# Kernel tuning notes

Hardware: AMD Instinct MI355X
Metric: run time of the kernel (lower is better)

## Reference

```python
import jax, jax.numpy as jnp
import numpy as np

N = 4096
FIN = 512
HID = 256
NCLS = 2
NE = 131072

def _glorot(key, fan_in, fan_out):
    r = np.sqrt(6.0 / (fan_in + fan_out))
    return jax.random.uniform(key, (fan_in, fan_out), jnp.float32, -r, r)

def setup_inputs() -> dict:
    key = jax.random.key(0)
    ks = jax.random.split(key, 16)
    X = jax.random.normal(ks[0], (N, FIN), jnp.float32)
    adj_rows = jax.random.randint(ks[1], (NE,), 0, N, jnp.int32)
    adj_cols = jax.random.randint(ks[2], (NE,), 0, N, jnp.int32)
    adj_vals = jax.random.uniform(ks[3], (NE,), jnp.float32)
    W_shared = _glorot(ks[4], FIN, HID)
    W_iv = _glorot(ks[5], HID, HID)
    W_c = _glorot(ks[6], HID, HID)
    W_r = _glorot(ks[7], HID, HID)
    Wg_iv = _glorot(ks[8], HID, HID)
    Wg_c = _glorot(ks[9], HID, HID)
    Wg_r = _glorot(ks[10], HID, HID)
    lin_W = _glorot(ks[11], 2 * HID, NCLS)
    lin_b = jnp.zeros((NCLS,), jnp.float32)
    return {"X": X, "adj_rows": adj_rows, "adj_cols": adj_cols, "adj_vals": adj_vals,
            "W_shared": W_shared, "W_iv": W_iv, "W_c": W_c, "W_r": W_r,
            "Wg_iv": Wg_iv, "Wg_c": Wg_c, "Wg_r": Wg_r, "lin_W": lin_W, "lin_b": lin_b}

def _spmm(rows, cols, vals, m):
    # sparse.mm(adj, m): out[i] = sum_{e: rows[e]==i} vals[e] * m[cols[e]]
    return jax.ops.segment_sum(vals[:, None] * m[cols], rows, num_segments=N)

def _gcn(x, rows, cols, vals, W):
    # dropout is identity in eval mode
    return jax.nn.relu(_spmm(rows, cols, vals, x @ W))

def _graphite(x, r1, r2, W):
    h = x @ W
    return jax.nn.relu(r1 @ (r1.T @ h) + r2 @ (r2.T @ h))

def reference(X, adj_rows, adj_cols, adj_vals, W_shared, W_iv, W_c, W_r, Wg_iv, Wg_c, Wg_r, lin_W, lin_b):
    h = _gcn(X, adj_rows, adj_cols, adj_vals, W_shared)
    z_iv0 = _gcn(h, adj_rows, adj_cols, adj_vals, W_iv)
    z_c0 = _gcn(h, adj_rows, adj_cols, adj_vals, W_c)
    z_r0 = _gcn(h, adj_rows, adj_cols, adj_vals, W_r)
    z_iv_rec0 = z_iv0 @ z_iv0.T
    z_c_rec0 = z_c0 @ z_c0.T
    z_r_rec0 = z_r0 @ z_r0.T
    A_dense = jnp.zeros((N, N), jnp.float32).at[adj_rows, adj_cols].add(adj_vals)
    z_iv = _graphite(z_iv0, A_dense, jax.nn.sigmoid(z_iv_rec0), Wg_iv)
    z_c = _graphite(z_c0, A_dense, jax.nn.sigmoid(z_c_rec0), Wg_c)
    z_r = _graphite(z_r0, A_dense, jax.nn.sigmoid(z_r_rec0), Wg_r)
    z_iv_rec = z_iv @ z_iv.T
    z_c_rec = z_c @ z_c.T
    z_r_rec = z_r @ z_r.T
    concat = jnp.concatenate([z_iv, z_c], axis=1)
    pred_T = jax.nn.log_softmax(concat @ lin_W + lin_b, axis=1)
    mi_total_loss = jnp.array(0.0, jnp.float32)
    return (z_iv, z_iv_rec, z_c, z_c_rec, z_r, z_r_rec, mi_total_loss, pred_T)
```

## Files before the change

### kernel.cpp

```cpp
#include <hip/hip_runtime.h>

#define Nn   4096
#define FINd 512
#define HIDd 256
#define NEd  131072

typedef unsigned short u16;
typedef __bf16 bf16x8 __attribute__((ext_vector_type(8)));
typedef float floatx4 __attribute__((ext_vector_type(4)));

__device__ __forceinline__ float bf2f(u16 u) {
  union { unsigned int i; float f; } v; v.i = ((unsigned int)u) << 16; return v.f;
}
__device__ __forceinline__ u16 f2bf(float f) {
  union { unsigned int i; float f; } v; v.f = f;
  unsigned int x = v.i;
  return (u16)((x + 0x7FFFu + ((x >> 16) & 1u)) >> 16);
}

#define GLDS(gp, lp) __builtin_amdgcn_global_load_lds( \
    (__attribute__((address_space(1))) unsigned int*)(void*)(gp), \
    (__attribute__((address_space(3))) unsigned int*)(lp), 16, 0, 0)

#define GATH4(EP, M, F, AX, AY, AZ, AW, E)                                     \
  {                                                                            \
    int2 c0 = (EP)[E]; int2 c1 = (EP)[(E) + 1];                                \
    int2 c2 = (EP)[(E) + 2]; int2 c3 = (EP)[(E) + 3];                          \
    ushort4 m0 = *(const ushort4*)((M) + (size_t)c0.x * HIDd + (F));           \
    ushort4 m1 = *(const ushort4*)((M) + (size_t)c1.x * HIDd + (F));           \
    ushort4 m2 = *(const ushort4*)((M) + (size_t)c2.x * HIDd + (F));           \
    ushort4 m3 = *(const ushort4*)((M) + (size_t)c3.x * HIDd + (F));           \
    float v0 = __int_as_float(c0.y), v1 = __int_as_float(c1.y);                \
    float v2 = __int_as_float(c2.y), v3 = __int_as_float(c3.y);                \
    AX = fmaf(v3, bf2f(m3.x), fmaf(v2, bf2f(m2.x), fmaf(v1, bf2f(m1.x), fmaf(v0, bf2f(m0.x), AX)))); \
    AY = fmaf(v3, bf2f(m3.y), fmaf(v2, bf2f(m2.y), fmaf(v1, bf2f(m1.y), fmaf(v0, bf2f(m0.y), AY)))); \
    AZ = fmaf(v3, bf2f(m3.z), fmaf(v2, bf2f(m2.z), fmaf(v1, bf2f(m1.z), fmaf(v0, bf2f(m0.z), AZ)))); \
    AW = fmaf(v3, bf2f(m3.w), fmaf(v2, bf2f(m2.w), fmaf(v1, bf2f(m1.w), fmaf(v0, bf2f(m0.w), AW)))); \
  }

#define GATH8(EP, M, F, AX, AY, AZ, AW, E)                                     \
  {                                                                            \
    int2 c0 = (EP)[E];       int2 c1 = (EP)[(E) + 1];                          \
    int2 c2 = (EP)[(E) + 2]; int2 c3 = (EP)[(E) + 3];                          \
    int2 c4 = (EP)[(E) + 4]; int2 c5 = (EP)[(E) + 5];                          \
    int2 c6 = (EP)[(E) + 6]; int2 c7 = (EP)[(E) + 7];                          \
    ushort4 m0 = *(const ushort4*)((M) + (size_t)c0.x * HIDd + (F));           \
    ushort4 m1 = *(const ushort4*)((M) + (size_t)c1.x * HIDd + (F));           \
    ushort4 m2 = *(const ushort4*)((M) + (size_t)c2.x * HIDd + (F));           \
    ushort4 m3 = *(const ushort4*)((M) + (size_t)c3.x * HIDd + (F));           \
    ushort4 m4 = *(const ushort4*)((M) + (size_t)c4.x * HIDd + (F));           \
    ushort4 m5 = *(const ushort4*)((M) + (size_t)c5.x * HIDd + (F));           \
    ushort4 m6 = *(const ushort4*)((M) + (size_t)c6.x * HIDd + (F));           \
    ushort4 m7 = *(const ushort4*)((M) + (size_t)c7.x * HIDd + (F));           \
    float v0 = __int_as_float(c0.y), v1 = __int_as_float(c1.y);                \
    float v2 = __int_as_float(c2.y), v3 = __int_as_float(c3.y);                \
    float v4 = __int_as_float(c4.y), v5 = __int_as_float(c5.y);                \
    float v6 = __int_as_float(c6.y), v7 = __int_as_float(c7.y);                \
    AX = fmaf(v7, bf2f(m7.x), fmaf(v6, bf2f(m6.x), fmaf(v5, bf2f(m5.x), fmaf(v4, bf2f(m4.x), \
         fmaf(v3, bf2f(m3.x), fmaf(v2, bf2f(m2.x), fmaf(v1, bf2f(m1.x), fmaf(v0, bf2f(m0.x), AX)))))))); \
    AY = fmaf(v7, bf2f(m7.y), fmaf(v6, bf2f(m6.y), fmaf(v5, bf2f(m5.y), fmaf(v4, bf2f(m4.y), \
         fmaf(v3, bf2f(m3.y), fmaf(v2, bf2f(m2.y), fmaf(v1, bf2f(m1.y), fmaf(v0, bf2f(m0.y), AY)))))))); \
    AZ = fmaf(v7, bf2f(m7.z), fmaf(v6, bf2f(m6.z), fmaf(v5, bf2f(m5.z), fmaf(v4, bf2f(m4.z), \
         fmaf(v3, bf2f(m3.z), fmaf(v2, bf2f(m2.z), fmaf(v1, bf2f(m1.z), fmaf(v0, bf2f(m0.z), AZ)))))))); \
    AW = fmaf(v7, bf2f(m7.w), fmaf(v6, bf2f(m6.w), fmaf(v5, bf2f(m5.w), fmaf(v4, bf2f(m4.w), \
         fmaf(v3, bf2f(m3.w), fmaf(v2, bf2f(m2.w), fmaf(v1, bf2f(m1.w), fmaf(v0, bf2f(m0.w), AW)))))))); \
  }

__global__ __launch_bounds__(256) void hist_priv_k(const int* __restrict__ rows,
                                                   const int* __restrict__ cols,
                                                   int* __restrict__ slabs) {
  __shared__ int cnt[8192];
  const int t = threadIdx.x;
  for (int i = t; i < 8192; i += 256) cnt[i] = 0;
  __syncthreads();
  int base = blockIdx.x * 1024;
  for (int i = t; i < 1024; i += 256) {
    int e = base + i;
    atomicAdd(&cnt[rows[e]], 1);
    atomicAdd(&cnt[4096 + cols[e]], 1);
  }
  __syncthreads();
  int* out = slabs + blockIdx.x * 8192;
  for (int i = t; i < 8192; i += 256) out[i] = cnt[i];
}

__global__ __launch_bounds__(256) void redslab_k(const int* __restrict__ slabs,
                                                 int* __restrict__ sums) {
  int bkt = blockIdx.x * 256 + threadIdx.x;
  int s = 0;
  for (int sl = 0; sl < 128; ++sl) s += slabs[sl * 8192 + bkt];
  sums[bkt] = s;
}

__global__ __launch_bounds__(1024) void scan2_k(const unsigned int* __restrict__ X,
                                                const int* __restrict__ sums,
                                                int* __restrict__ rp, int* __restrict__ cp,
                                                int* __restrict__ rfill, int* __restrict__ cfill,
                                                int* __restrict__ flag) {
  __shared__ int part[1024];
  __shared__ int dcnt;
  const int t = threadIdx.x;
  if (t == 0) dcnt = 0;
  __syncthreads();
  int local = 0;
  for (int i = t; i < 4096; i += 1024) {
    unsigned e = (X[i] >> 7) & 0xFFu;
    if (e >= 100u && e <= 140u) local++;
  }
  if (local) atomicAdd(&dcnt, local);
  int base = t * 8, s = 0, loc[8];
  int csum[8];
#pragma unroll
  for (int j = 0; j < 8; ++j) csum[j] = sums[base + j];
#pragma unroll
  for (int j = 0; j < 8; ++j) { loc[j] = s; s += csum[j]; }
  part[t] = s;
  __syncthreads();
  if (t == 0) *flag = (dcnt > 2458) ? 1 : 0;
  for (int off = 1; off < 1024; off <<= 1) {
    int v = (t >= off) ? part[t - off] : 0;
    __syncthreads();
    part[t] += v;
    __syncthreads();
  }
  int excl = (t == 0) ? 0 : part[t - 1];
  int rtot = part[511];
  if (t < 512) {
#pragma unroll
    for (int j = 0; j < 8; ++j) rp[base + j] = excl + loc[j];
    if (t == 511) rp[4096] = rtot;
  } else {
    int cb = base - 4096;
    int ex2 = excl - rtot;
#pragma unroll
    for (int j = 0; j < 8; ++j) cp[cb + j] = ex2 + loc[j];
    if (t == 1023) cp[4096] = part[1023] - rtot;
  }
  for (int i = t; i < 4096; i += 1024) { rfill[i] = 0; cfill[i] = 0; }
}

__global__ __launch_bounds__(256) void setup2_k(const void* __restrict__ X,
                                                const void* __restrict__ Wsh,
                                                const void* __restrict__ W0, const void* __restrict__ W1,
                                                const void* __restrict__ W2, const void* __restrict__ G0,
                                                const void* __restrict__ G1, const void* __restrict__ G2,
                                                const void* __restrict__ linW, const void* __restrict__ linb,
                                                const int* __restrict__ rows, const int* __restrict__ cols,
                                                const void* __restrict__ vals,
                                                const int* __restrict__ rp, const int* __restrict__ cp,
                                                int* __restrict__ rfill, int* __restrict__ cfill,
                                                int2* __restrict__ rpack, int2* __restrict__ cpack,
                                                u16* __restrict__ Xb, u16* __restrict__ WshT,
                                                u16* __restrict__ WTb, u16* __restrict__ WgTb,
                                                float* __restrict__ linWf, float* __restrict__ linbf,
                                                const int* __restrict__ flag) {
  int fl = *flag;
  int bx = blockIdx.x;
  if (bx >= 10245) {
    int e = (bx - 10245) * 256 + threadIdx.x;
    if (e >= NEd) return;
    float v = fl ? bf2f(((const u16*)vals)[e]) : ((const float*)vals)[e];
    int r = rows[e], c = cols[e];
    int p1 = rp[r] + atomicAdd(&rfill[r], 1);
    rpack[p1] = make_int2(c, __float_as_int(v));
    int p2 = cp[c] + atomicAdd(&cfill[c], 1);
    cpack[p2] = make_int2(r, __float_as_int(v));
    return;
  }
  int i = bx * 256 + threadIdx.x;
  if (i < 2097152) {
    Xb[i] = fl ? ((const u16*)X)[i] : f2bf(((const float*)X)[i]);
    return;
  }
  int i2 = i - 2097152;
  if (i2 < 131072) {
    int r = i2 >> 8, c = i2 & 255;
    u16 v = fl ? ((const u16*)Wsh)[i2] : f2bf(((const float*)Wsh)[i2]);
    WshT[c * 512 + r] = v;
    return;
  }
  int i3 = i2 - 131072;
  if (i3 < 393216) {
    int w = i3 >> 16, j = i3 & 65535;
    int r = j >> 8, c = j & 255;
    const void* src = (w == 0) ? W0 : (w == 1) ? W1 : (w == 2) ? W2
                     : (w == 3) ? G0 : (w == 4) ? G1 : G2;
    u16 v = fl ? ((const u16*)src)[j] : f2bf(((const float*)src)[j]);
    u16* dst = (w < 3) ? (WTb + w * 65536) : (WgTb + (w - 3) * 65536);
    dst[c * 256 + r] = v;
    return;
  }
  int i4 = i3 - 393216;
  if (i4 < 1024) { linWf[i4] = fl ? bf2f(((const u16*)linW)[i4]) : ((const float*)linW)[i4]; return; }
  if (i4 < 1026) { int k = i4 - 1024; linbf[k] = fl ? bf2f(((const u16*)linb)[k]) : ((const float*)linb)[k]; }
}

struct SPP {
  const int* ptr; const int2* ep;
  const u16* m[3]; u16* ob[3]; unsigned long long oo[3];
};
__global__ __launch_bounds__(256) void spmm_mb_k(SPP s, const float* __restrict__ part,
                                                 void* __restrict__ outbase, int mode,
                                                 const int* __restrict__ flag) {
  const int b = blockIdx.y;
  int gid = blockIdx.x * 256 + threadIdx.x;
  int row = gid >> 6, lane = gid & 63, f = lane << 2;
  int beg = s.ptr[row], end = s.ptr[row + 1];
  const u16* m = s.m[b];
  float ax = 0.f, ay = 0.f, az = 0.f, aw = 0.f;
  int e = beg;
  for (; e + 7 < end; e += 8) GATH8(s.ep, m, f, ax, ay, az, aw, e);
  for (; e + 3 < end; e += 4) GATH4(s.ep, m, f, ax, ay, az, aw, e);
  for (; e < end; ++e) {
    int2 cv = s.ep[e];
    float v = __int_as_float(cv.y);
    ushort4 mv = *(const ushort4*)(m + (size_t)cv.x * HIDd + f);
    ax = fmaf(v, bf2f(mv.x), ax);
    ay = fmaf(v, bf2f(mv.y), ay);
    az = fmaf(v, bf2f(mv.z), az);
    aw = fmaf(v, bf2f(mv.w), aw);
  }
  size_t o = (size_t)row * HIDd + f;
  if (mode == 2) {
    const float* pb = part + (size_t)b * 1048576 + o;
    float4 p0 = *(const float4*)(pb);
    float4 p1 = *(const float4*)(pb + 3145728);
    float4 p2 = *(const float4*)(pb + 2 * 3145728);
    float4 p3 = *(const float4*)(pb + 3 * 3145728);
    ax += p0.x + p1.x + p2.x + p3.x;
    ay += p0.y + p1.y + p2.y + p3.y;
    az += p0.z + p1.z + p2.z + p3.z;
    aw += p0.w + p1.w + p2.w + p3.w;
    ax = fmaxf(ax, 0.f); ay = fmaxf(ay, 0.f);
    az = fmaxf(az, 0.f); aw = fmaxf(aw, 0.f);
    ushort4 o4 = { f2bf(ax), f2bf(ay), f2bf(az), f2bf(aw) };
    *(ushort4*)(s.ob[b] + o) = o4;
    if (*flag) *(ushort4*)((u16*)outbase + s.oo[b] + o) = o4;
    else       *(float4*)((float*)outbase + s.oo[b] + o) = make_float4(ax, ay, az, aw);
  } else {
    if (mode == 0) {
      ax = fmaxf(ax, 0.f); ay = fmaxf(ay, 0.f);
      az = fmaxf(az, 0.f); aw = fmaxf(aw, 0.f);
    }
    ushort4 o4 = { f2bf(ax), f2bf(ay), f2bf(az), f2bf(aw) };
    *(ushort4*)(s.ob[b] + o) = o4;
  }
}

__global__ __launch_bounds__(256) void redt_k(const float* __restrict__ part,
                                              u16* __restrict__ tT) {
  int i = (blockIdx.x * 256 + threadIdx.x) * 4;
  float4 s0 = *(const float4*)(part + i);
  float4 s1 = *(const float4*)(part + i + 3145728);
  float4 s2 = *(const float4*)(part + i + 2 * 3145728);
  float4 s3 = *(const float4*)(part + i + 3 * 3145728);
  ushort4 o = { f2bf(s0.x + s1.x + s2.x + s3.x), f2bf(s0.y + s1.y + s2.y + s3.y),
                f2bf(s0.z + s1.z + s2.z + s3.z), f2bf(s0.w + s1.w + s2.w + s3.w) };
  *(ushort4*)(tT + i) = o;
}

struct TQ {
  const u16* Ap[3]; const u16* Bp[3]; unsigned long long c0[3];
  int tallA, K, N, kspan;
  const int* cp; const int2* cep;
  const u16* hp[3]; u16* ub[3];
};

__global__ __launch_bounds__(512) void tall_spmmu_k(TQ P, float* __restrict__ partf) {
  __shared__ __align__(16) u16 smem[24576];
  const int b = blockIdx.z;
  const int bx = blockIdx.x;
  if (bx >= 128) {
    int gid = (bx - 128) * 512 + threadIdx.x;
    int row = gid >> 6, lane = gid & 63, f = lane << 2;
    int beg = P.cp[row], end = P.cp[row + 1];
    const u16* m = P.hp[b];
    float ax = 0.f, ay = 0.f, az = 0.f, aw = 0.f;
    int e = beg;
    for (; e + 3 < end; e += 4) GATH4(P.cep, m, f, ax, ay, az, aw, e);
    for (; e < end; ++e) {
      int2 cv = P.cep[e];
      float v = __int_as_float(cv.y);
      ushort4 mv = *(const ushort4*)(m + (size_t)cv.x * HIDd + f);
      ax = fmaf(v, bf2f(mv.x), ax);
      ay = fmaf(v, bf2f(mv.y), ay);
      az = fmaf(v, bf2f(mv.z), az);
      aw = fmaf(v, bf2f(mv.w), aw);
    }
    size_t o = (size_t)row * HIDd + f;
    ushort4 o4 = { f2bf(ax), f2bf(ay), f2bf(az), f2bf(aw) };
    *(ushort4*)(P.ub[b] + o) = o4;
    return;
  }
  const u16* A = P.Ap[b];
  const u16* B = P.Bp[b];
  const int K = P.K, N = P.N, tallA = P.tallA;
  const int stripe = bx & 31, ks = bx >> 5;
  const int tid = threadIdx.x, w = tid >> 6, lane = tid & 63;
  const int lr = lane >> 3, cc = lane & 7;
  const int scol = (cc ^ lr) << 3;
  u16* As = smem;
  u16* Bs = smem + (tallA ? 16384 : 8192);
  int wrow, wcol;
  if (tallA) { wrow = (w >> 1) * 64; wcol = (w & 1) * 64; }
  else       { wrow = (w >> 2) * 64; wcol = (w & 3) * 64; }
  const int row0 = tallA ? 0 : stripe * 128;
  const int col0 = tallA ? stripe * 128 : 0;
  const int na = tallA ? 4 : 2;
  const int nb = tallA ? 2 : 4;
  floatx4 acc[4][4] = {};
  int aoff[4], boff[4];
#pragma unroll
  for (int i = 0; i < 4; ++i) {
    int m = wrow + i * 16 + (lane & 15);
    aoff[i] = m * 64 + (((lane >> 4) << 3) ^ ((m & 7) << 3));
    int n = wcol + i * 16 + (lane & 15);
    boff[i] = n * 64 + (((lane >> 4) << 3) ^ ((n & 7) << 3));
  }
  const int kbeg = ks * P.kspan, kend = kbeg + P.kspan;
  for (int k0 = kbeg; k0 < kend; k0 += 64) {
#pragma unroll
    for (int t = 0; t < 4; ++t) {
      if (t < na) {
        int ch = na * w + t;
        GLDS(A + (size_t)(row0 + 8 * ch + lr) * K + k0 + scol, As + ch * 512);
      }
      if (t < nb) {
        int ch = nb * w + t;
        GLDS(B + (size_t)(col0 + 8 * ch + lr) * K + k0 + scol, Bs + ch * 512);
      }
    }
    __syncthreads();
#pragma unroll
    for (int kk = 0; kk < 2; ++kk) {
      bf16x8 af[4], bfr[4];
#pragma unroll
      for (int i = 0; i < 4; ++i) {
        af[i]  = *(const bf16x8*)(As + (aoff[i] ^ (kk << 5)));
        bfr[i] = *(const bf16x8*)(Bs + (boff[i] ^ (kk << 5)));
      }
#pragma unroll
      for (int i = 0; i < 4; ++i)
#pragma unroll
        for (int j = 0; j < 4; ++j)
          acc[i][j] = __builtin_amdgcn_mfma_f32_16x16x32_bf16(af[i], bfr[j], acc[i][j], 0, 0, 0);
    }
    __syncthreads();
  }
  const int l15 = lane & 15, q4 = (lane >> 4) << 2;
  float* C = partf + P.c0[b] + (size_t)ks * 3145728;
  const int cbase = col0 + wcol + l15;
#pragma unroll
  for (int i = 0; i < 4; ++i)
#pragma unroll
    for (int r = 0; r < 4; ++r) {
      size_t rb = (size_t)(row0 + wrow + i * 16 + q4 + r) * N + cbase;
#pragma unroll
      for (int j = 0; j < 4; ++j) C[rb + j * 16] = acc[i][j][r];
    }
}

struct Job {
  const u16* A; const u16* B;
  const float* F1; const float* F2;
  unsigned long long c0, c1, pstride;
  int M, N, K, mode, xt, ntiles, nks, kspan, sym;
};
struct Jobs { Job j[6]; };

__global__ __launch_bounds__(256) void gemm_mega(Jobs P, void* __restrict__ WSv,
                                                 void* __restrict__ OutO,
                                                 const int* __restrict__ flag) {
  __shared__ __align__(16) u16 smem[17408];
  u16* As = smem;
  u16* Bs = smem + 8192;
  u16* Ts = smem;
  const Job jb = P.j[blockIdx.z];
  const unsigned tile = blockIdx.x;
  if ((int)tile >= jb.ntiles * jb.nks) return;
  if (jb.mode == 6) {
    int i = tile * 256 + threadIdx.x;
    const float* lw = jb.F1;
    float a0 = jb.F2[0], a1 = jb.F2[1];
    for (int f = 0; f < HIDd; ++f) {
      float zv = bf2f(jb.A[(size_t)i * HIDd + f]);
      a0 = fmaf(zv, lw[2 * f + 0], a0);
      a1 = fmaf(zv, lw[2 * f + 1], a1);
    }
    for (int f = 0; f < HIDd; ++f) {
      float zv = bf2f(jb.B[(size_t)i * HIDd + f]);
      a0 = fmaf(zv, lw[2 * (HIDd + f) + 0], a0);
      a1 = fmaf(zv, lw[2 * (HIDd + f) + 1], a1);
    }
    float mx = fmaxf(a0, a1);
    float lse = mx + logf(expf(a0 - mx) + expf(a1 - mx));
    float p0 = a0 - lse, p1 = a1 - lse;
    if (*flag) {
      u16* ob = (u16*)OutO;
      ob[jb.c0 + 2 * i + 0] = f2bf(p0);
      ob[jb.c0 + 2 * i + 1] = f2bf(p1);
      if (i == 0) ob[jb.c1] = 0;
    } else {
      float* ob = (float*)OutO;
      ob[jb.c0 + 2 * i + 0] = p0;
      ob[jb.c0 + 2 * i + 1] = p1;
      if (i == 0) ob[jb.c1] = 0.f;
    }
    return;
  }
  const unsigned ks = tile / (unsigned)jb.ntiles;
  const unsigned t2 = tile - ks * jb.ntiles;
  unsigned ty, tx;
  if (jb.sym) {
    unsigned rem = t2, rowlen = jb.xt; ty = 0;
    while (rem >= rowlen) { rem -= rowlen; --rowlen; ++ty; }
    tx = ty + rem;
  } else {
    ty = t2 / (unsigned)jb.xt;
    tx = t2 - ty * jb.xt;
  }
  const int K = jb.K, N = jb.N;
  const int row0 = ty * 128, col0 = tx * 128;
  const int tid = threadIdx.x;
  const int w = tid >> 6, lane = tid & 63;
  const int wr = (w >> 1) * 64, wc = (w & 1) * 64;
  const int lr = lane >> 3, cc = lane & 7;
  const int scol = (cc ^ lr) << 3;
  floatx4 acc[4][4] = {};
  int aoff[4], boff[4];
#pragma unroll
  for (int i = 0; i < 4; ++i) {
    int m = wr + i * 16 + (lane & 15);
    aoff[i] = m * 64 + ((((lane >> 4) << 3)) ^ ((m & 7) << 3));
    int n = wc + i * 16 + (lane & 15);
    boff[i] = n * 64 + ((((lane >> 4) << 3)) ^ ((n & 7) << 3));
  }
  const u16* A = jb.A;
  const u16* B = jb.B;
  const int kbeg = ks * jb.kspan, kend = kbeg + jb.kspan;
  for (int k0 = kbeg; k0 < kend; k0 += 64) {
#pragma unroll
    for (int t = 0; t < 4; ++t) {
      int ch = 4 * w + t;
      GLDS(A + (size_t)(row0 + 8 * ch + lr) * K + k0 + scol, As + ch * 512);
      GLDS(B + (size_t)(col0 + 8 * ch + lr) * K + k0 + scol, Bs + ch * 512);
    }
    __syncthreads();
#pragma unroll
    for (int kk = 0; kk < 2; ++kk) {
      bf16x8 af[4], bfr[4];
#pragma unroll
      for (int i = 0; i < 4; ++i) {
        af[i]  = *(const bf16x8*)(As + (aoff[i] ^ (kk << 5)));
        bfr[i] = *(const bf16x8*)(Bs + (boff[i] ^ (kk << 5)));
      }
#pragma unroll
      for (int i = 0; i < 4; ++i)
#pragma unroll
        for (int j = 0; j < 4; ++j)
          acc[i][j] = __builtin_amdgcn_mfma_f32_16x16x32_bf16(af[i], bfr[j], acc[i][j], 0, 0, 0);
    }
    __syncthreads();
  }

  const int l15 = lane & 15, q4 = (lane >> 4) << 2;
  const int cb = col0 + wc + l15;
  const int mode = jb.mode;
  if (mode == 0 || mode == 1) {
    u16* C = ((mode == 1) ? (u16*)OutO : (u16*)WSv) + jb.c0;
#pragma unroll
    for (int i = 0; i < 4; ++i)
#pragma unroll
      for (int r = 0; r < 4; ++r) {
        int lrow = wr + i * 16 + q4 + r;
        size_t rb = (size_t)(row0 + lrow) * N + cb;
#pragma unroll
        for (int j = 0; j < 4; ++j) {
          float v = acc[i][j][r];
          if (mode == 1) v = 1.f / (1.f + __expf(-v));
          u16 vb = f2bf(v);
          C[rb + j * 16] = vb;
          if (jb.sym) Ts[(wc + j * 16 + l15) * 136 + lrow] = vb;
        }
      }
    if (jb.sym && tx != ty) {
      __syncthreads();
      int rr = tid >> 1, hf = (tid & 1) << 6;
      size_t rb2 = (size_t)(col0 + rr) * N + row0 + hf;
#pragma unroll
      for (int k = 0; k < 8; ++k)
        *(uint4*)(C + rb2 + k * 8) = *(const uint4*)(Ts + rr * 136 + hf + k * 8);
    }
  } else if (mode == 4) {
    u16* C  = (u16*)WSv + jb.c0;
    u16* CT = (u16*)WSv + jb.c1;
    const int M = jb.M;
#pragma unroll
    for (int i = 0; i < 4; ++i)
#pragma unroll
      for (int r = 0; r < 4; ++r) {
        int gr = row0 + wr + i * 16 + q4 + r;
#pragma unroll
        for (int j = 0; j < 4; ++j) {
          u16 v = f2bf(acc[i][j][r]);
          int gc = cb + j * 16;
          C[(size_t)gr * N + gc] = v;
          CT[(size_t)gc * M + gr] = v;
        }
      }
  } else {
    if (*flag) {
      u16* C = (u16*)OutO + jb.c0;
#pragma unroll
      for (int i = 0; i < 4; ++i)
#pragma unroll
        for (int r = 0; r < 4; ++r) {
          int lrow = wr + i * 16 + q4 + r;
          size_t rb = (size_t)(row0 + lrow) * N + cb;
#pragma unroll
          for (int j = 0; j < 4; ++j) {
            u16 vb = f2bf(acc[i][j][r]);
            C[rb + j * 16] = vb;
            if (jb.sym) Ts[(wc + j * 16 + l15) * 136 + lrow] = vb;
          }
        }
      if (jb.sym && tx != ty) {
        __syncthreads();
        int rr = tid >> 1, hf = (tid & 1) << 6;
        size_t rb2 = (size_t)(col0 + rr) * N + row0 + hf;
#pragma unroll
        for (int k = 0; k < 8; ++k)
          *(uint4*)(C + rb2 + k * 8) = *(const uint4*)(Ts + rr * 136 + hf + k * 8);
      }
    } else {
      float* C = (float*)OutO + jb.c0;
#pragma unroll
      for (int i = 0; i < 4; ++i)
#pragma unroll
      for (int r = 0; r < 4; ++r) {
          int gr = row0 + wr + i * 16 + q4 + r;
          size_t rb = (size_t)gr * N + cb;
#pragma unroll
          for (int j = 0; j < 4; ++j) C[rb + j * 16] = acc[i][j][r];
        }
      if (jb.sym && tx != ty) {
        float* Tf = (float*)smem;
        const int whalf = w & 1;
#pragma unroll
        for (int half = 0; half < 2; ++half) {
          __syncthreads();
          if (whalf == half) {
#pragma unroll
            for (int i = 0; i < 4; ++i)
#pragma unroll
              for (int j = 0; j < 4; ++j) {
                int cl = j * 16 + l15;
#pragma unroll
                for (int r = 0; r < 4; ++r)
                  Tf[cl * 132 + wr + i * 16 + q4 + r] = acc[i][j][r];
              }
          }
          __syncthreads();
          int cl = tid >> 2, chf = (tid & 3) << 5;
          size_t rb2 = (size_t)(col0 + half * 64 + cl) * N + row0 + chf;
          const float* src = Tf + cl * 132 + chf;
#pragma unroll
          for (int k = 0; k < 8; ++k)
            *(float4*)(C + rb2 + k * 4) = *(const float4*)(src + k * 4);
        }
      }
    }
  }
}

extern "C" void kernel_launch(void* const* d_in, const int* in_sizes, int n_in,
                              void* d_out, int out_size, void* d_ws, size_t ws_size,
                              hipStream_t stream) {
  const void* X    = d_in[0];
  const int*  rows = (const int*)d_in[1];
  const int*  cols = (const int*)d_in[2];
  const void* vals = d_in[3];
  const void* Wsh  = d_in[4];

  char* W = (char*)d_ws;
  u16*  Xb    = (u16*)(W + 0);
  u16*  WshT  = (u16*)(W + 4194304);
  u16*  WTb   = (u16*)(W + 4456448);
  u16*  WgTb  = (u16*)(W + 4849664);
  int*  rp    = (int*)(W + 5242880);
  int*  cp    = (int*)(W + 5275648);
  int*  rfill = (int*)(W + 5308416);
  int*  cfill = (int*)(W + 5324800);
  int2* rpack = (int2*)(W + 5341184);
  int2* cpack = (int2*)(W + 6389760);
  float* linWf = (float*)(W + 7438336);
  float* linbf = (float*)(W + 7442432);
  int*  flag  = (int*)(W + 7442560);
  u16*  hb    = (u16*)(W + 8388608);
  u16*  tmpb[3] = { (u16*)(W + 10485760), (u16*)(W + 12582912), (u16*)(W + 14680064) };
  u16*  z0b[3]  = { (u16*)(W + 16777216), (u16*)(W + 18874368), (u16*)(W + 20971520) };
  u16*  hpb[3]  = { (u16*)(W + 23068672), (u16*)(W + 25165824), (u16*)(W + 27262976) };
  u16*  hpT[3]  = { (u16*)(W + 29360128), (u16*)(W + 31457280), (u16*)(W + 33554432) };
  u16*  tTb     = (u16*)(W + 35651584);
  u16*  zbb[3]  = { (u16*)(W + 41943040), (u16*)(W + 44040192), (u16*)(W + 46137344) };
  u16*  ubb[3]  = { (u16*)(W + 48234496), (u16*)(W + 50331648), (u16*)(W + 52428800) };
  float* partf  = (float*)(W + 54525952);
  int*  slabs  = (int*)(W + 54525952);
  int*  sums   = (int*)(W + 54525952 + 4194304);

  const long long z_off[3]   = { 0LL, 17825792LL, 35651584LL };
  const long long rec_off[3] = { 1048576LL, 18874368LL, 36700160LL };
  const long long mi_off = 53477376LL, pred_off = 53477377LL;

  const u16* r2p[3] = { (const u16*)d_out + rec_off[0], (const u16*)d_out + rec_off[1],
                        (const u16*)d_out + rec_off[2] };

  hist_priv_k<<<128, 256, 0, stream>>>(rows, cols, slabs);
  redslab_k<<<32, 256, 0, stream>>>(slabs, sums);
  scan2_k<<<1, 1024, 0, stream>>>((const unsigned int*)X, sums, rp, cp, rfill, cfill, flag);
  setup2_k<<<10757, 256, 0, stream>>>(X, Wsh, d_in[5], d_in[6], d_in[7],
                                      d_in[8], d_in[9], d_in[10], d_in[11], d_in[12],
                                      rows, cols, vals, rp, cp, rfill, cfill, rpack, cpack,
                                      Xb, WshT, WTb, WgTb, linWf, linbf, flag);

  Jobs P{};
  auto setj = [](Job& j, const u16* A, const u16* B, unsigned long long c0,
                 unsigned long long c1, unsigned long long ps, int M, int N, int K,
                 int mode, int nks, int sym) {
    j.A = A; j.B = B; j.F1 = nullptr; j.F2 = nullptr;
    j.c0 = c0; j.c1 = c1; j.pstride = ps;
    j.M = M; j.N = N; j.K = K; j.mode = mode;
    j.xt = N / 128;
    j.ntiles = sym ? (j.xt * (j.xt + 1)) / 2 : (M / 128) * (N / 128);
    j.nks = nks; j.kspan = K / nks; j.sym = sym;
  };

  setj(P.j[0], Xb, WshT, ((char*)tmpb[0] - W) / 2, 0, 0, Nn, HIDd, FINd, 0, 1, 0);
  gemm_mega<<<dim3(64, 1, 1), 256, 0, stream>>>(P, d_ws, d_out, flag);

  SPP s{};
  s.ptr = rp; s.ep = rpack;
  s.m[0] = tmpb[0]; s.ob[0] = hb;
  spmm_mb_k<<<dim3(Nn / 4, 1), 256, 0, stream>>>(s, nullptr, nullptr, 0, flag);

  for (int b = 0; b < 3; ++b)
    setj(P.j[b], hb, WTb + b * 65536, ((char*)tmpb[b] - W) / 2, 0, 0, Nn, HIDd, HIDd, 0, 1, 0);
  gemm_mega<<<dim3(64, 1, 3), 256, 0, stream>>>(P, d_ws, d_out, flag);

  for (int b = 0; b < 3; ++b) { s.m[b] = tmpb[b]; s.ob[b] = z0b[b]; }
  spmm_mb_k<<<dim3(Nn / 4, 3), 256, 0, stream>>>(s, nullptr, nullptr, 0, flag);

  for (int b = 0; b < 3; ++b) {
    setj(P.j[b], z0b[b], z0b[b], rec_off[b], 0, 0, Nn, Nn, HIDd, 1, 1, 1);
    setj(P.j[3 + b], z0b[b], WgTb + b * 65536, ((char*)hpb[b] - W) / 2,
         ((char*)hpT[b] - W) / 2, 0, Nn, HIDd, HIDd, 4, 1, 0);
  }
  gemm_mega<<<dim3(528, 1, 6), 256, 0, stream>>>(P, d_ws, d_out, flag);

  TQ T{};
  for (int b = 0; b < 3; ++b) {
    T.Ap[b] = hpT[b]; T.Bp[b] = r2p[b];
    T.c0[b] = (unsigned long long)b * 1048576ULL;
    T.hp[b] = hpb[b]; T.ub[b] = ubb[b];
  }
  T.tallA = 1; T.K = Nn; T.N = Nn; T.kspan = 1024;
  T.cp = cp; T.cep = cpack;
  tall_spmmu_k<<<dim3(640, 1, 3), 512, 0, stream>>>(T, partf);

  redt_k<<<3072, 256, 0, stream>>>(partf, tTb);

  TQ T2{};
  for (int b = 0; b < 3; ++b) {
    T2.Ap[b] = r2p[b]; T2.Bp[b] = tTb + b * 1048576;
    T2.c0[b] = (unsigned long long)b * 1048576ULL;
    T2.hp[b] = nullptr; T2.ub[b] = nullptr;
  }
  T2.tallA = 0; T2.K = Nn; T2.N = HIDd; T2.kspan = 1024;
  T2.cp = nullptr; T2.cep = nullptr;
  tall_spmmu_k<<<dim3(128, 1, 3), 512, 0, stream>>>(T2, partf);

  for (int b = 0; b < 3; ++b) {
    s.m[b] = ubb[b];
    s.ob[b] = zbb[b]; s.oo[b] = (unsigned long long)z_off[b];
  }
  spmm_mb_k<<<dim3(Nn / 4, 3), 256, 0, stream>>>(s, partf, d_out, 2, flag);

  for (int b = 0; b < 3; ++b)
    setj(P.j[b], zbb[b], zbb[b], rec_off[b], 0, 0, Nn, Nn, HIDd, 3, 1, 1);
  setj(P.j[3], zbb[0], zbb[1], (unsigned long long)pred_off,
       (unsigned long long)mi_off, 0, 256, 128, 64, 6, 1, 0);
  P.j[3].ntiles = 16; P.j[3].nks = 1;
  P.j[3].F1 = linWf; P.j[3].F2 = linbf;
  gemm_mega<<<dim3(528, 1, 4), 256, 0, stream>>>(P, d_ws, d_out, flag);

  (void)in_sizes; (void)n_in; (void)out_size; (void)ws_size;
}
```

Baseline: 605.4 us.

## Route second graphite GEMM through tiled MFMA mega-kernel with split-K partials

Replaces the tall_spmmu_k launch for the r2 @ (r2^T h) product with a new gemm_mega mode 5. Mode 5 runs 128x128 MFMA tiles with a 4-way K split and writes fp32 partial sums into the partf workspace for the downstream reduction. It also remaps tile indices so that consecutive workgroups interleave across K-splits, likely to spread work across XCDs and caches. The cost is writing fp32 partials through the generic GEMM path, whose per-tile efficiency for this shape is not guaranteed.

```diff
diff --git a/kernel.cpp b/kernel.cpp
--- a/kernel.cpp
+++ b/kernel.cpp
@@ -376,7 +376,7 @@
   u16* Bs = smem + 8192;
   u16* Ts = smem;
   const Job jb = P.j[blockIdx.z];
-  const unsigned tile = blockIdx.x;
+  unsigned tile = blockIdx.x;
   if ((int)tile >= jb.ntiles * jb.nks) return;
   if (jb.mode == 6) {
     int i = tile * 256 + threadIdx.x;
@@ -408,6 +408,11 @@
     }
     return;
   }
+  if (jb.mode == 5) {
+    unsigned nwg = (unsigned)(jb.ntiles * jb.nks);
+    unsigned q = nwg >> 3;
+    tile = (tile & 7u) * q + (tile >> 3);
+  }
   const unsigned ks = tile / (unsigned)jb.ntiles;
   const unsigned t2 = tile - ks * jb.ntiles;
   unsigned ty, tx;
@@ -466,7 +471,17 @@
   const int l15 = lane & 15, q4 = (lane >> 4) << 2;
   const int cb = col0 + wc + l15;
   const int mode = jb.mode;
-  if (mode == 0 || mode == 1) {
+  if (mode == 5) {
+    float* C = (float*)WSv + jb.c0 + (size_t)ks * jb.pstride;
+#pragma unroll
+    for (int i = 0; i < 4; ++i)
+#pragma unroll
+      for (int r = 0; r < 4; ++r) {
+        size_t rb = (size_t)(row0 + wr + i * 16 + q4 + r) * N + cb;
+#pragma unroll
+        for (int j = 0; j < 4; ++j) C[rb + j * 16] = acc[i][j][r];
+      }
+  } else if (mode == 0 || mode == 1) {
     u16* C = ((mode == 1) ? (u16*)OutO : (u16*)WSv) + jb.c0;
 #pragma unroll
     for (int i = 0; i < 4; ++i)
@@ -607,6 +622,7 @@
   float* partf  = (float*)(W + 54525952);
   int*  slabs  = (int*)(W + 54525952);
   int*  sums   = (int*)(W + 54525952 + 4194304);
+  const unsigned long long part_e0 = 54525952ULL / 4;
 
   const long long z_off[3]   = { 0LL, 17825792LL, 35651584LL };
   const long long rec_off[3] = { 1048576LL, 18874368LL, 36700160LL };
@@ -669,15 +685,10 @@
 
   redt_k<<<3072, 256, 0, stream>>>(partf, tTb);
 
-  TQ T2{};
-  for (int b = 0; b < 3; ++b) {
-    T2.Ap[b] = r2p[b]; T2.Bp[b] = tTb + b * 1048576;
-    T2.c0[b] = (unsigned long long)b * 1048576ULL;
-    T2.hp[b] = nullptr; T2.ub[b] = nullptr;
-  }
-  T2.tallA = 0; T2.K = Nn; T2.N = HIDd; T2.kspan = 1024;
-  T2.cp = nullptr; T2.cep = nullptr;
-  tall_spmmu_k<<<dim3(128, 1, 3), 512, 0, stream>>>(T2, partf);
+  for (int b = 0; b < 3; ++b)
+    setj(P.j[b], r2p[b], tTb + b * 1048576, part_e0 + (unsigned long long)b * 1048576, 0,
+         3145728, Nn, HIDd, Nn, 5, 4, 0);
+  gemm_mega<<<dim3(256, 1, 3), 256, 0, stream>>>(P, d_ws, d_out, flag);
 
   for (int b = 0; b < 3; ++b) {
     s.m[b] = ubb[b];
```

Result: no change. 611.5 us (+1.0%).
